# Performance work log

Measured on AMD Instinct MI355X. Metric: run time of the kernel, lower is better.

## Reference

```python
import jax, jax.numpy as jnp
import numpy as np

N = 100000
E = 1600000
IN, HID, OUT = 512, 256, 32
K = 3
LAMBDA_AMP = 0.5


def setup_inputs() -> dict:
    key = jax.random.key(0)
    ks = jax.random.split(key, 6)
    x = jax.random.normal(ks[0], (N, IN), dtype=jnp.float32)
    edge_index = jax.random.randint(ks[1], (2, E), 0, N, dtype=jnp.int64)
    # MLP params (PyTorch Linear default init: U(-1/sqrt(fan_in), 1/sqrt(fan_in)))
    s1 = 1.0 / np.sqrt(IN)
    W1 = jax.random.uniform(ks[2], (IN, HID), jnp.float32, -s1, s1)
    b1 = jax.random.uniform(ks[3], (HID,), jnp.float32, -s1, s1)
    s2 = 1.0 / np.sqrt(HID)
    W2 = jax.random.uniform(ks[4], (HID, OUT), jnp.float32, -s2, s2)
    b2 = jax.random.uniform(ks[5], (OUT,), jnp.float32, -s2, s2)
    return {"x": x, "W1": W1, "b1": b1, "W2": W2, "b2": b2, "edge_index": edge_index}


def _gcn_norm(edge_index, n_nodes, dtype):
    # add self loops, symmetric normalization D^-1/2 (A+I) D^-1/2
    loop = jnp.arange(n_nodes, dtype=edge_index.dtype)
    row = jnp.concatenate([edge_index[0], loop])
    col = jnp.concatenate([edge_index[1], loop])
    w = jnp.ones(row.shape[0], dtype=dtype)
    deg = jax.ops.segment_sum(w, col, num_segments=n_nodes)
    dis = jnp.where(deg > 0, jax.lax.rsqrt(deg), 0.0)
    norm = dis[row] * w * dis[col]
    return row, col, norm


def _proximal_l21(x, lam):
    # row-wise soft-thresholding of L2 norms
    rn = jnp.sqrt(jnp.sum(x * x, axis=1))  # [N]
    safe = jnp.where(rn > 0, rn, 1.0)
    score = jnp.where(rn > 0, jnp.maximum(rn - lam, 0.0) / safe, 0.0)
    return score[:, None] * x


def reference(x, W1, b1, W2, b2, edge_index):
    # MLP (dropout inactive at inference)
    h = jax.nn.relu(x @ W1 + b1)
    h = h @ W2 + b2  # [N, OUT]

    row, col, norm = _gcn_norm(edge_index, N, h.dtype)

    lam = LAMBDA_AMP
    gamma = 1.0 / (2.0 * (1.0 - lam))
    hh = h
    xk = h
    for _ in range(K):
        # A_hat @ xk via gather-scale-scatter
        ax = jax.ops.segment_sum(norm[:, None] * xk[row], col, num_segments=N)
        lx = xk - ax  # L @ xk
        y = xk - gamma * 2.0 * (1.0 - lam) * lx
        xk = hh + _proximal_l21(y - hh, lam * gamma)
    return xk
```

## Files before the change

kernel.cpp:

```cpp
#include <hip/hip_runtime.h>
#include <cstdint>

#define NN 100000
#define EE 1600000
#define IN_F 512
#define HID_F 256
#define OUT_F 32
#define GSL 256
#define SLICE_W 12500
#define CAP 64

typedef float f32x4 __attribute__((ext_vector_type(4)));
typedef int   i32x4 __attribute__((ext_vector_type(4)));
typedef short s16x8 __attribute__((ext_vector_type(8)));
typedef uint32_t u32x4 __attribute__((ext_vector_type(4)));
typedef unsigned short u16;

static __device__ __forceinline__ u16 f2bf(float f) {
  uint32_t u = __builtin_bit_cast(uint32_t, f);
  u += 0x7FFFu + ((u >> 16) & 1u);
  return (u16)(u >> 16);
}

static __device__ __forceinline__ float bf2f(u16 v) {
  uint32_t u = ((uint32_t)v) << 16;
  return __builtin_bit_cast(float, u);
}

static __device__ __forceinline__ uint32_t pk_bf16(float a, float b) {
  uint32_t r;
  asm("v_cvt_pk_bf16_f32 %0, %1, %2" : "=v"(r) : "v"(a), "v"(b));
  return r;
}

__global__ __launch_bounds__(256) void k_prep(const float* __restrict__ w1,
                                              u16* __restrict__ w1f,
                                              const float* __restrict__ w2,
                                              u16* __restrict__ w2f,
                                              int* __restrict__ cur) {
  int b = blockIdx.x;
  int tid = threadIdx.x;
  if (b < 512) {
    int g = b * 256 + tid;
    int j    = g & 7;
    int lane = (g >> 3) & 63;
    int fnG  = (g >> 9) & 15;
    int kk   = g >> 13;
    int k = kk * 32 + (lane >> 4) * 8 + j;
    int n = fnG * 16 + (lane & 15);
    w1f[g] = f2bf(w1[k * HID_F + n]);
  } else if (b < 544) {
    int g = (b - 512) * 256 + tid;
    int j    = g & 7;
    int lane = (g >> 3) & 63;
    int ff   = g >> 9;
    int k = (ff >> 1) * 32 + (lane >> 4) * 8 + j;
    int n = (ff & 1) * 16 + (lane & 15);
    w2f[g] = f2bf(w2[k * OUT_F + n]);
  } else {
    int i = (b - 544) * 256 + tid;
    if (i < NN) cur[i] = 0;
  }
}

__global__ __launch_bounds__(256) void k_fillC(const int* __restrict__ row,
                                               const int* __restrict__ col,
                                               int* __restrict__ cur,
                                               int* __restrict__ csr) {
  const int slice = blockIdx.x & 7;
  const int g = blockIdx.x >> 3;
  const unsigned lo = (unsigned)slice * SLICE_W, hi = lo + SLICE_W;
  const i32x4* c4 = (const i32x4*)col;
  const i32x4* r4 = (const i32x4*)row;
  for (int i = g * 256 + threadIdx.x; i < EE / 4; i += GSL * 256) {
    i32x4 c = c4[i];
    i32x4 r = r4[i];
    #pragma unroll
    for (int k = 0; k < 4; ++k) {
      unsigned cc = (unsigned)c[k];
      if (cc >= lo && cc < hi) {
        int p = atomicAdd(&cur[cc], 1);
        if (p < CAP) csr[(int)cc * CAP + p] = r[k];
      }
    }
  }
}

__global__ __launch_bounds__(512) void k_mlp(
    const float* __restrict__ x, const float* __restrict__ b1,
    const float* __restrict__ b2, const u16* __restrict__ w1f,
    const u16* __restrict__ w2f, const int* __restrict__ cnt,
    float* __restrict__ hout, u16* __restrict__ xs0) {
  __shared__ char smem[65536];
  char* aL0 = smem;
  char* aL1 = smem + 16384;
  char* h1L = smem;

  const int tid  = threadIdx.x;
  const int lane = tid & 63;
  const int wid  = tid >> 6;
  const int wm   = wid >> 2;
  const int wn   = wid & 3;
  const int l16  = lane & 15;
  const int lq   = lane >> 4;
  const int row0 = blockIdx.x * 128;

  const f32x4 zf = {0.f, 0.f, 0.f, 0.f};

  auto loadA = [&](int kt, f32x4 ar[4]) {
    #pragma unroll
    for (int p = 0; p < 4; ++p) {
      int v   = p * 512 + tid;
      int row = v >> 4;
      int f4  = v & 15;
      int grow = row0 + row;
      ar[p] = zf;
      if (grow < NN)
        ar[p] = *(const f32x4*)(x + (size_t)grow * IN_F + kt * 64 + f4 * 4);
    }
  };
  auto writeA = [&](char* buf, f32x4 ar[4]) {
    #pragma unroll
    for (int p = 0; p < 4; ++p) {
      int v   = p * 512 + tid;
      int row = v >> 4;
      int f4  = v & 15;
      uint32_t lo = pk_bf16(ar[p].x, ar[p].y);
      uint32_t hi = pk_bf16(ar[p].z, ar[p].w);
      uint64_t wv = (uint64_t)lo | ((uint64_t)hi << 32);
      int kb = (f4 * 8) ^ ((row & 7) << 4);
      *(uint64_t*)(buf + row * 128 + kb) = wv;
    }
  };

  f32x4 acc[4][4];
  #pragma unroll
  for (int i = 0; i < 4; ++i)
    #pragma unroll
    for (int j = 0; j < 4; ++j) acc[i][j] = zf;

  f32x4 ar[4];
  loadA(0, ar);
  writeA(aL0, ar);

  #pragma unroll
  for (int kt = 0; kt < IN_F / 64; ++kt) {
    char* aCur = (kt & 1) ? aL1 : aL0;
    char* aNxt = (kt & 1) ? aL0 : aL1;
    __syncthreads();
    if (kt < 7) loadA(kt + 1, ar);
    #pragma unroll
    for (int ks = 0; ks < 2; ++ks) {
      const int kk = kt * 2 + ks;
      s16x8 af[4], bf[4];
      #pragma unroll
      for (int fn = 0; fn < 4; ++fn)
        bf[fn] = *(const s16x8*)(w1f + ((size_t)(kk * 16 + wn * 4 + fn) * 64 + lane) * 8);
      #pragma unroll
      for (int fm = 0; fm < 4; ++fm) {
        int row = wm * 64 + fm * 16 + l16;
        int kb  = (ks * 64 + lq * 16) ^ ((row & 7) << 4);
        af[fm] = *(const s16x8*)(aCur + row * 128 + kb);
      }
      #pragma unroll
      for (int fm = 0; fm < 4; ++fm)
        #pragma unroll
        for (int fn = 0; fn < 4; ++fn)
          acc[fm][fn] = __builtin_amdgcn_mfma_f32_16x16x32_bf16(
              af[fm], bf[fn], acc[fm][fn], 0, 0, 0);
    }
    if (kt < 7) writeA(aNxt, ar);
  }

  float b1v[4];
  #pragma unroll
  for (int fn = 0; fn < 4; ++fn) b1v[fn] = b1[wn * 64 + fn * 16 + l16];

  __syncthreads();
  #pragma unroll
  for (int fm = 0; fm < 4; ++fm) {
    #pragma unroll
    for (int fn = 0; fn < 4; ++fn) {
      int col = wn * 64 + fn * 16 + l16;
      #pragma unroll
      for (int r = 0; r < 4; ++r) {
        int row = wm * 64 + fm * 16 + lq * 4 + r;
        float v = acc[fm][fn][r] + b1v[fn];
        v = fmaxf(v, 0.f);
        *(u16*)(h1L + row * 512 + ((col * 2) ^ ((row & 7) << 4))) = f2bf(v);
      }
    }
  }
  __syncthreads();

  f32x4 acc2[2];
  acc2[0] = zf; acc2[1] = zf;
  const int arow = wid * 16 + l16;
  #pragma unroll
  for (int ks = 0; ks < 8; ++ks) {
    int kb = ks * 64 + lq * 16;
    s16x8 af = *(const s16x8*)(h1L + arow * 512 + (kb ^ ((arow & 7) << 4)));
    #pragma unroll
    for (int fn = 0; fn < 2; ++fn) {
      s16x8 bfr = *(const s16x8*)(w2f + ((size_t)((ks * 2 + fn) * 64) + lane) * 8);
      acc2[fn] = __builtin_amdgcn_mfma_f32_16x16x32_bf16(af, bfr, acc2[fn], 0, 0, 0);
    }
  }
  #pragma unroll
  for (int r = 0; r < 4; ++r) {
    int row = row0 + wid * 16 + lq * 4 + r;
    if (row >= NN) continue;
    float dr = rsqrtf((float)cnt[row] + 1.0f);
    #pragma unroll
    for (int fn = 0; fn < 2; ++fn) {
      int col = fn * 16 + l16;
      float v = acc2[fn][r] + b2[col];
      hout[(size_t)row * 32 + col] = v;
      xs0[(size_t)row * 32 + col] = f2bf(dr * v);
    }
  }
}

template <int LAST>
__global__ __launch_bounds__(256) void k_prop(
    const u16* __restrict__ xs, const float* __restrict__ hh,
    u16* __restrict__ xs_out, float* __restrict__ fout,
    const int* __restrict__ cnt, const int* __restrict__ csr) {
  int w = blockIdx.x * 4 + (threadIdx.x >> 6);
  if (w >= NN) return;
  const int lane = threadIdx.x & 63;
  const int q = lane & 3;
  const int s = lane >> 2;
  const int n = cnt[w];
  const int* __restrict__ crow = csr + (size_t)w * CAP;
  float acc[8] = {0.f, 0.f, 0.f, 0.f, 0.f, 0.f, 0.f, 0.f};
  for (int j = s; j < n; j += 16) {
    int src = crow[j];
    s16x8 v = *(const s16x8*)(xs + (size_t)src * 32 + q * 8);
    #pragma unroll
    for (int k = 0; k < 8; ++k) acc[k] += bf2f((u16)v[k]);
  }
  if (s == 0) {
    s16x8 v = *(const s16x8*)(xs + (size_t)w * 32 + q * 8);
    #pragma unroll
    for (int k = 0; k < 8; ++k) acc[k] += bf2f((u16)v[k]);
  }
  #pragma unroll
  for (int m = 4; m <= 32; m <<= 1) {
    #pragma unroll
    for (int k = 0; k < 8; ++k) acc[k] += __shfl_xor(acc[k], m, 64);
  }
  const float di = rsqrtf((float)n + 1.0f);
  const f32x4 h0 = *(const f32x4*)(hh + (size_t)w * 32 + q * 8);
  const f32x4 h1 = *(const f32x4*)(hh + (size_t)w * 32 + q * 8 + 4);
  float hv[8] = {h0.x, h0.y, h0.z, h0.w, h1.x, h1.y, h1.z, h1.w};
  float d[8];
  float rn2 = 0.f;
  #pragma unroll
  for (int k = 0; k < 8; ++k) {
    d[k] = di * acc[k] - hv[k];
    rn2 += d[k] * d[k];
  }
  rn2 += __shfl_xor(rn2, 1, 64);
  rn2 += __shfl_xor(rn2, 2, 64);
  float rn = sqrtf(rn2);
  float sc = (rn > 0.f) ? fmaxf(rn - 0.5f, 0.f) / rn : 0.f;
  if (s == 0) {
    if (LAST) {
      f32x4 o0, o1;
      o0.x = hv[0] + sc * d[0]; o0.y = hv[1] + sc * d[1];
      o0.z = hv[2] + sc * d[2]; o0.w = hv[3] + sc * d[3];
      o1.x = hv[4] + sc * d[4]; o1.y = hv[5] + sc * d[5];
      o1.z = hv[6] + sc * d[6]; o1.w = hv[7] + sc * d[7];
      *(f32x4*)(fout + (size_t)w * 32 + q * 8) = o0;
      *(f32x4*)(fout + (size_t)w * 32 + q * 8 + 4) = o1;
    } else {
      s16x8 o;
      #pragma unroll
      for (int k = 0; k < 8; ++k) o[k] = (short)f2bf(di * (hv[k] + sc * d[k]));
      *(s16x8*)(xs_out + (size_t)w * 32 + q * 8) = o;
    }
  }
}

extern "C" void kernel_launch(void* const* d_in, const int* in_sizes, int n_in,
                              void* d_out, int out_size, void* d_ws, size_t ws_size,
                              hipStream_t stream) {
  const float* x  = (const float*)d_in[0];
  const float* W1 = (const float*)d_in[1];
  const float* b1 = (const float*)d_in[2];
  const float* W2 = (const float*)d_in[3];
  const float* b2 = (const float*)d_in[4];
  const int*   ei = (const int*)d_in[5];

  char* ws = (char*)d_ws;
  float* h    = (float*)(ws);
  u16*   xs0  = (u16*)  (ws + 12800000);
  u16*   xs1  = (u16*)  (ws + 19200000);
  int*   csr  = (int*)  (ws + 25600000);
  int*   cur  = (int*)  (ws + 51200000);
  u16*   w1f  = (u16*)  (ws + 51600000);
  u16*   w2f  = (u16*)  (ws + 51862144);

  k_prep<<<935, 256, 0, stream>>>(W1, w1f, W2, w2f, cur);
  k_fillC<<<8 * GSL, 256, 0, stream>>>(ei, ei + EE, cur, csr);
  k_mlp<<<(NN + 127) / 128, 512, 0, stream>>>(x, b1, b2, w1f, w2f, cur, h, xs0);

  float* out = (float*)d_out;
  k_prop<0><<<(NN + 3) / 4, 256, 0, stream>>>(xs0, h, xs1, nullptr, cur, csr);
  k_prop<0><<<(NN + 3) / 4, 256, 0, stream>>>(xs1, h, xs0, nullptr, cur, csr);
  k_prop<1><<<(NN + 3) / 4, 256, 0, stream>>>(xs0, h, nullptr, out,  cur, csr);
}
```

Baseline: 284.2 us.

## Load MLP input tiles directly into LDS via global_load_lds, convert to bf16 on read

Replaces the register-staged, double-buffered A-tile path (global load to VGPRs, bf16 convert, LDS write) with direct global-to-LDS DMA loads of fp32 data in a single buffer. The fp32-to-bf16 conversion moves to the LDS read side, just before the MFMAs. This cuts VGPR pressure and the store instructions, but drops the software prefetch overlap. Each fp32 tile is twice the LDS bytes, and every wave now repeats the conversion work on its reads.

```diff
diff --git a/kernel.cpp b/kernel.cpp
--- a/kernel.cpp
+++ b/kernel.cpp
@@ -31,6 +31,12 @@
   uint32_t r;
   asm("v_cvt_pk_bf16_f32 %0, %1, %2" : "=v"(r) : "v"(a), "v"(b));
   return r;
+}
+
+static __device__ __forceinline__ void gload_lds16(const float* g, void* l) {
+  __builtin_amdgcn_global_load_lds(
+      (const __attribute__((address_space(1))) uint32_t*)g,
+      (__attribute__((address_space(3))) uint32_t*)l, 16, 0, 0);
 }
 
 __global__ __launch_bounds__(256) void k_prep(const float* __restrict__ w1,
@@ -92,8 +98,7 @@
     const u16* __restrict__ w2f, const int* __restrict__ cnt,
     float* __restrict__ hout, u16* __restrict__ xs0) {
   __shared__ char smem[65536];
-  char* aL0 = smem;
-  char* aL1 = smem + 16384;
+  char* aL  = smem;
   char* h1L = smem;
 
   const int tid  = threadIdx.x;
@@ -106,49 +111,33 @@
   const int row0 = blockIdx.x * 128;
 
   const f32x4 zf = {0.f, 0.f, 0.f, 0.f};
-
-  auto loadA = [&](int kt, f32x4 ar[4]) {
+  f32x4 acc[4][4];
+  #pragma unroll
+  for (int i = 0; i < 4; ++i)
+    #pragma unroll
+    for (int j = 0; j < 4; ++j) acc[i][j] = zf;
+
+  int srow[4], sgc[4];
+  #pragma unroll
+  for (int p = 0; p < 4; ++p) {
+    int v   = p * 512 + tid;
+    int row = v >> 4;
+    srow[p] = row;
+    int grow = row0 + row;
+    if (grow >= NN) grow = NN - 1;
+    sgc[p] = grow;
+  }
+
+  for (int kt = 0; kt < IN_F / 64; ++kt) {
+    __syncthreads();
     #pragma unroll
     for (int p = 0; p < 4; ++p) {
-      int v   = p * 512 + tid;
-      int row = v >> 4;
-      int f4  = v & 15;
-      int grow = row0 + row;
-      ar[p] = zf;
-      if (grow < NN)
-        ar[p] = *(const f32x4*)(x + (size_t)grow * IN_F + kt * 64 + f4 * 4);
-    }
-  };
-  auto writeA = [&](char* buf, f32x4 ar[4]) {
-    #pragma unroll
-    for (int p = 0; p < 4; ++p) {
-      int v   = p * 512 + tid;
-      int row = v >> 4;
-      int f4  = v & 15;
-      uint32_t lo = pk_bf16(ar[p].x, ar[p].y);
-      uint32_t hi = pk_bf16(ar[p].z, ar[p].w);
-      uint64_t wv = (uint64_t)lo | ((uint64_t)hi << 32);
-      int kb = (f4 * 8) ^ ((row & 7) << 4);
-      *(uint64_t*)(buf + row * 128 + kb) = wv;
-    }
-  };
-
-  f32x4 acc[4][4];
-  #pragma unroll
-  for (int i = 0; i < 4; ++i)
-    #pragma unroll
-    for (int j = 0; j < 4; ++j) acc[i][j] = zf;
-
-  f32x4 ar[4];
-  loadA(0, ar);
-  writeA(aL0, ar);
-
-  #pragma unroll
-  for (int kt = 0; kt < IN_F / 64; ++kt) {
-    char* aCur = (kt & 1) ? aL1 : aL0;
-    char* aNxt = (kt & 1) ? aL0 : aL1;
+      int row = srow[p];
+      int c   = (lane & 15) ^ (row & 15);
+      const float* g = x + (size_t)sgc[p] * IN_F + kt * 64 + c * 4;
+      gload_lds16(g, aL + (p * 512 + wid * 64) * 16);
+    }
     __syncthreads();
-    if (kt < 7) loadA(kt + 1, ar);
     #pragma unroll
     for (int ks = 0; ks < 2; ++ks) {
       const int kk = kt * 2 + ks;
@@ -159,8 +148,17 @@
       #pragma unroll
       for (int fm = 0; fm < 4; ++fm) {
         int row = wm * 64 + fm * 16 + l16;
-        int kb  = (ks * 64 + lq * 16) ^ ((row & 7) << 4);
-        af[fm] = *(const s16x8*)(aCur + row * 128 + kb);
+        int c0  = ks * 8 + lq * 2;
+        int p0  = c0 ^ (row & 15);
+        int p1  = (c0 + 1) ^ (row & 15);
+        f32x4 v0 = *(const f32x4*)(aL + row * 256 + p0 * 16);
+        f32x4 v1 = *(const f32x4*)(aL + row * 256 + p1 * 16);
+        u32x4 pk;
+        pk.x = pk_bf16(v0.x, v0.y);
+        pk.y = pk_bf16(v0.z, v0.w);
+        pk.z = pk_bf16(v1.x, v1.y);
+        pk.w = pk_bf16(v1.z, v1.w);
+        af[fm] = __builtin_bit_cast(s16x8, pk);
       }
       #pragma unroll
       for (int fm = 0; fm < 4; ++fm)
@@ -169,7 +167,6 @@
           acc[fm][fn] = __builtin_amdgcn_mfma_f32_16x16x32_bf16(
               af[fm], bf[fn], acc[fm][fn], 0, 0, 0);
     }
-    if (kt < 7) writeA(aNxt, ar);
   }
 
   float b1v[4];
```

Measured after the change: 304.9 us. 1.07x slower.
